# Kernel optimization log

Hardware: AMD Instinct MI355X
Metric: run time of the kernel (lower is better)

Reference implementation:

```python
import jax, jax.numpy as jnp
import numpy as np

N = 100000
E = 800000

def elu(x):
    return jnp.where(x > 0, x, jnp.expm1(x))

def transformer_conv(x, src, dst, ea, Wq, bq, Wk, bk, Wv, bv, We, Ws, bs, heads, ch):
    # PyG TransformerConv (concat=True, root_weight=True, beta=False, eval so dropout off)
    n = x.shape[0]
    q = (x @ Wq + bq).reshape(n, heads, ch)
    k = (x @ Wk + bk).reshape(n, heads, ch)
    v = (x @ Wv + bv).reshape(n, heads, ch)
    e = (ea @ We).reshape(-1, heads, ch)            # [E,H,C], lin_edge has no bias
    kj = k[src] + e                                  # [E,H,C]
    logits = (q[dst] * kj).sum(-1) / jnp.sqrt(jnp.float32(ch))  # [E,H]
    # segment softmax over incoming edges of each dst node
    m = jax.ops.segment_max(logits, dst, num_segments=n)
    ex = jnp.exp(logits - m[dst])
    denom = jax.ops.segment_sum(ex, dst, num_segments=n)
    alpha = ex / denom[dst]                          # [E,H]
    msg = alpha[..., None] * (v[src] + e)            # [E,H,C]
    agg = jax.ops.segment_sum(msg, dst, num_segments=n).reshape(n, heads * ch)
    return agg + x @ Ws + bs                         # skip connection (lin_skip)

def setup_inputs() -> dict:
    key = jax.random.key(0)
    ks = jax.random.split(key, 32)
    def rn(k, shape, scale=0.1):
        return jax.random.normal(k, shape, dtype=jnp.float32) * scale
    d = {}
    d['x'] = jax.random.normal(ks[0], (N, 23), dtype=jnp.float32)
    d['edge_index'] = jax.random.randint(ks[1], (2, E), 0, N, dtype=jnp.int32)
    d['edge_attr'] = jax.random.normal(ks[2], (E, 7), dtype=jnp.float32)
    d['linA_w'] = rn(ks[3], (23, 23)); d['linA_b'] = jnp.zeros((23,), jnp.float32)
    d['linB_w'] = rn(ks[4], (23, 23)); d['linB_b'] = jnp.zeros((23,), jnp.float32)
    # conv1: in=23, heads=8, out=24 -> 192
    d['q1_w'] = rn(ks[5], (23, 192)); d['q1_b'] = jnp.zeros((192,), jnp.float32)
    d['k1_w'] = rn(ks[6], (23, 192)); d['k1_b'] = jnp.zeros((192,), jnp.float32)
    d['v1_w'] = rn(ks[7], (23, 192)); d['v1_b'] = jnp.zeros((192,), jnp.float32)
    d['e1_w'] = rn(ks[8], (7, 192))
    d['s1_w'] = rn(ks[9], (23, 192)); d['s1_b'] = jnp.zeros((192,), jnp.float32)
    # conv4: in=192, heads=8, out=8 -> 64
    d['q2_w'] = rn(ks[10], (192, 64)); d['q2_b'] = jnp.zeros((64,), jnp.float32)
    d['k2_w'] = rn(ks[11], (192, 64)); d['k2_b'] = jnp.zeros((64,), jnp.float32)
    d['v2_w'] = rn(ks[12], (192, 64)); d['v2_b'] = jnp.zeros((64,), jnp.float32)
    d['e2_w'] = rn(ks[13], (7, 64))
    d['s2_w'] = rn(ks[14], (192, 64)); d['s2_b'] = jnp.zeros((64,), jnp.float32)
    d['lin1_w'] = rn(ks[15], (64, 20)); d['lin1_b'] = jnp.zeros((20,), jnp.float32)
    d['lin2_w'] = rn(ks[16], (20, 1)); d['lin2_b'] = jnp.zeros((1,), jnp.float32)
    return d

def reference(x, edge_index, edge_attr,
              linA_w, linA_b, linB_w, linB_b,
              q1_w, q1_b, k1_w, k1_b, v1_w, v1_b, e1_w, s1_w, s1_b,
              q2_w, q2_b, k2_w, k2_b, v2_w, v2_b, e2_w, s2_w, s2_b,
              lin1_w, lin1_b, lin2_w, lin2_b):
    src, dst = edge_index[0], edge_index[1]
    h = elu(x @ linA_w + linA_b)
    h = elu(h @ linB_w + linB_b)
    h = transformer_conv(h, src, dst, edge_attr, q1_w, q1_b, k1_w, k1_b, v1_w, v1_b, e1_w, s1_w, s1_b, 8, 24)
    h = elu(h)
    h = transformer_conv(h, src, dst, edge_attr, q2_w, q2_b, k2_w, k2_b, v2_w, v2_b, e2_w, s2_w, s2_b, 8, 8)
    h = elu(h)
    h = elu(h @ lin1_w + lin1_b)
    return h @ lin2_w + lin2_b
```

## Files before the change

### kernel.cpp

```cpp
#include <hip/hip_runtime.h>
#include <math.h>


__device__ __forceinline__ float elu_f(float x) {
    return x > 0.f ? x : expm1f(x);
}


__global__ void mlp_kernel(const float* __restrict__ x,
                           const float* __restrict__ A, const float* __restrict__ ab,
                           const float* __restrict__ B, const float* __restrict__ bb,
                           float* __restrict__ out, int n) {
    __shared__ float sA[23 * 23], sB[23 * 23], sa[23], sb[23];
    for (int t = threadIdx.x; t < 23 * 23; t += blockDim.x) { sA[t] = A[t]; sB[t] = B[t]; }
    if (threadIdx.x < 23) { sa[threadIdx.x] = ab[threadIdx.x]; sb[threadIdx.x] = bb[threadIdx.x]; }
    __syncthreads();
    int i = blockIdx.x * blockDim.x + threadIdx.x;
    if (i >= n) return;
    float xi[23], h1[23];
    #pragma unroll
    for (int j = 0; j < 23; j++) xi[j] = x[(size_t)i * 23 + j];
    #pragma unroll
    for (int o = 0; o < 23; o++) {
        float acc = sa[o];
        #pragma unroll
        for (int j = 0; j < 23; j++) acc = fmaf(xi[j], sA[j * 23 + o], acc);
        h1[o] = elu_f(acc);
    }
    #pragma unroll
    for (int o = 0; o < 23; o++) {
        float acc = sb[o];
        #pragma unroll
        for (int j = 0; j < 23; j++) acc = fmaf(h1[j], sB[j * 23 + o], acc);
        out[(size_t)i * 23 + o] = elu_f(acc);
    }
}

template<int IN, int Kc, int OUTW, int M, int TY, bool FUSED>
__global__ void proj_tiled_kernel(const float* __restrict__ in, int n,
    const float* __restrict__ W0, const float* __restrict__ b0, float* __restrict__ o0,
    const float* __restrict__ W1, const float* __restrict__ b1, float* __restrict__ o1,
    const float* __restrict__ W2, const float* __restrict__ b2, float* __restrict__ o2,
    const float* __restrict__ W3, const float* __restrict__ b3, float* __restrict__ o3) {
    constexpr int WTOT = M * OUTW;
    constexpr int CG   = WTOT / 8;
    constexpr int BN   = TY * 4;
    constexpr int SAW  = BN + 4;
    constexpr int NT   = CG * TY;
    static_assert(IN % Kc == 0, "Kc must divide IN");
    static_assert(WTOT % 8 == 0 && OUTW % 4 == 0, "col alignment");
    __shared__ float sA[Kc][SAW];
    __shared__ float sB[Kc][WTOT];

    const int tid = threadIdx.x;
    const int tx = tid % CG;
    const int ty = tid / CG;
    const int node0 = blockIdx.x * BN;

    const int colA = tx * 4;
    const int colB = WTOT / 2 + tx * 4;
    const int matA = colA / OUTW, ccA = colA % OUTW;
    const int matB = colB / OUTW, ccB = colB % OUTW;
    const float* bA = (matA == 0 ? b0 : matA == 1 ? b1 : matA == 2 ? b2 : b3);
    const float* bB = (matB == 0 ? b0 : matB == 1 ? b1 : matB == 2 ? b2 : b3);
    float*       oA = (matA == 0 ? o0 : matA == 1 ? o1 : matA == 2 ? o2 : o3);
    float*       oB = (matB == 0 ? o0 : matB == 1 ? o1 : matB == 2 ? o2 : o3);

    float acc[4][8];
    #pragma unroll
    for (int i = 0; i < 4; i++) {
        #pragma unroll
        for (int c = 0; c < 4; c++) { acc[i][c] = bA[ccA + c]; acc[i][4 + c] = bB[ccB + c]; }
    }

    for (int k0 = 0; k0 < IN; k0 += Kc) {
        for (int t = tid; t < Kc * BN; t += NT) {
            int j = t / BN, nn = t - j * BN;
            int g = node0 + nn;
            sA[j][nn] = (g < n) ? in[(size_t)g * IN + k0 + j] : 0.f;
        }
        for (int t = tid; t < Kc * WTOT; t += NT) {
            int j = t / WTOT, c = t - j * WTOT;
            int m = c / OUTW, cm = c - m * OUTW;
            const float* Wp = (m == 0 ? W0 : m == 1 ? W1 : m == 2 ? W2 : W3);
            sB[j][c] = Wp[(size_t)(k0 + j) * OUTW + cm];
        }
        __syncthreads();
        #pragma unroll 8
        for (int j = 0; j < Kc; j++) {
            float4 a  = *(const float4*)&sA[j][ty * 4];
            float4 v0 = *(const float4*)&sB[j][colA];
            float4 v1 = *(const float4*)&sB[j][colB];
            float av[4] = {a.x, a.y, a.z, a.w};
            float bv[8] = {v0.x, v0.y, v0.z, v0.w, v1.x, v1.y, v1.z, v1.w};
            #pragma unroll
            for (int i = 0; i < 4; i++)
                #pragma unroll
                for (int c = 0; c < 8; c++)
                    acc[i][c] = fmaf(av[i], bv[c], acc[i][c]);
        }
        __syncthreads();
    }

    #pragma unroll
    for (int i = 0; i < 4; i++) {
        int g = node0 + ty * 4 + i;
        if (g >= n) continue;
        if constexpr (FUSED) {
            *(float4*)(o0 + (size_t)g * WTOT + colA) = make_float4(acc[i][0], acc[i][1], acc[i][2], acc[i][3]);
            *(float4*)(o0 + (size_t)g * WTOT + colB) = make_float4(acc[i][4], acc[i][5], acc[i][6], acc[i][7]);
        } else {
            *(float4*)(oA + (size_t)g * OUTW + ccA) = make_float4(acc[i][0], acc[i][1], acc[i][2], acc[i][3]);
            *(float4*)(oB + (size_t)g * OUTW + ccB) = make_float4(acc[i][4], acc[i][5], acc[i][6], acc[i][7]);
        }
    }
}


__global__ void zero2_kernel(int* __restrict__ a, int* __restrict__ b, int n) {
    int i = blockIdx.x * blockDim.x + threadIdx.x;
    if (i < n) { a[i] = 0; b[i] = 0; }
}

__global__ void count_kernel(const int* __restrict__ dst, int* __restrict__ cnt, int nE) {
    int e = blockIdx.x * blockDim.x + threadIdx.x;
    if (e < nE) atomicAdd(&cnt[dst[e]], 1);
}

__global__ void scan_block_kernel(int* __restrict__ cnt, int* __restrict__ bsum, int n) {
    __shared__ int sdat[256];
    int i = blockIdx.x * 256 + threadIdx.x;
    int v = (i < n) ? cnt[i] : 0;
    sdat[threadIdx.x] = v;
    __syncthreads();
    for (int off = 1; off < 256; off <<= 1) {
        int t = (threadIdx.x >= (unsigned)off) ? sdat[threadIdx.x - off] : 0;
        __syncthreads();
        sdat[threadIdx.x] += t;
        __syncthreads();
    }
    if (i < n) cnt[i] = sdat[threadIdx.x] - v;
    if (threadIdx.x == 255) bsum[blockIdx.x] = sdat[255];
}

__global__ void scan_bsum_kernel(int* __restrict__ bsum, int nb) {
    __shared__ int s[1024];
    int i = threadIdx.x;
    int v = (i < nb) ? bsum[i] : 0;
    s[i] = v;
    __syncthreads();
    for (int off = 1; off < 1024; off <<= 1) {
        int t = (i >= off) ? s[i - off] : 0;
        __syncthreads();
        s[i] += t;
        __syncthreads();
    }
    if (i < nb) bsum[i] = s[i] - v;
}

__global__ void finalize_rp_kernel(const int* __restrict__ cnt, const int* __restrict__ bsum,
                                   int* __restrict__ rp, int n, int nE) {
    int i = blockIdx.x * blockDim.x + threadIdx.x;
    if (i < n) rp[i] = cnt[i] + bsum[i >> 8];
    if (i == n) rp[n] = nE;
}

__global__ void scatter_kernel(const int* __restrict__ src, const int* __restrict__ dst,
                               const int* __restrict__ rp, int* __restrict__ cur,
                               int2* __restrict__ seS, int nE) {
    int e = blockIdx.x * blockDim.x + threadIdx.x;
    if (e >= nE) return;
    int d = dst[e];
    int pos = rp[d] + atomicAdd(&cur[d], 1);
    seS[pos] = make_int2(src[e], e);
}

template<int IN, int C, bool VMAT, bool QMAT, bool DOELU>
__global__ __launch_bounds__(256, 8)
void conv_fused_kernel(const float* __restrict__ feat,
                       const float* __restrict__ Wq, const float* __restrict__ qb,
                       const float* __restrict__ Wv, const float* __restrict__ vb,
                       const float* __restrict__ kmat, const float* __restrict__ qmat,
                       const float* __restrict__ ea, const float* __restrict__ We,
                       const int* __restrict__ rp, const int2* __restrict__ seS,
                       float* __restrict__ out, int n, float scale, int chunk) {
    constexpr int HC = 8 * C;
    constexpr int CPL = HC / 64;
    __shared__ float sWv[VMAT ? 1 : IN * HC];
    if constexpr (!VMAT) {
        for (int t = threadIdx.x; t < IN * HC; t += blockDim.x) sWv[t] = Wv[t];
        __syncthreads();
    }
    const int lane = threadIdx.x & 63;
    const int wid = (blockIdx.x * blockDim.x + threadIdx.x) >> 6;
    const int d0 = wid * chunk;
    const int dEnd = min(n, d0 + chunk);
    if (d0 >= dEnd) return;
    const int ch0 = lane * CPL;

    float we[7][CPL];
    #pragma unroll
    for (int j = 0; j < 7; j++)
        #pragma unroll
        for (int c = 0; c < CPL; c++) we[j][c] = We[j * HC + ch0 + c];

    float vbr[CPL];
    if constexpr (!VMAT) {
        #pragma unroll
        for (int c = 0; c < CPL; c++) vbr[c] = vb[ch0 + c];
    }

    for (int d = d0; d < dEnd; d++) {
        float q[CPL];
        if constexpr (QMAT) {
            const float* qp = qmat + (size_t)d * HC + ch0;
            #pragma unroll
            for (int c = 0; c < CPL; c++) q[c] = qp[c];
        } else {
            #pragma unroll
            for (int c = 0; c < CPL; c++) q[c] = qb[ch0 + c];
            const float* fd = feat + (size_t)d * IN;
            for (int j = 0; j < IN; j++) {
                float f = fd[j];
                #pragma unroll
                for (int c = 0; c < CPL; c++)
                    q[c] = fmaf(f, Wq[(size_t)j * HC + ch0 + c], q[c]);
            }
        }

        float m = -INFINITY, l = 0.f, acc[CPL];
        #pragma unroll
        for (int c = 0; c < CPL; c++) acc[c] = 0.f;

        const int p0 = rp[d], p1 = rp[d + 1];

        if constexpr (VMAT) {
            if (p0 < p1) {
                int2 se0 = seS[p0];
                int sU = __builtin_amdgcn_readfirstlane(se0.x);
                int eU = __builtin_amdgcn_readfirstlane(se0.y);
                float ec[7];
                {
                    const float* ep = ea + (size_t)eU * 7;
                    #pragma unroll
                    for (int j = 0; j < 7; j++) ec[j] = ep[j];
                }
                for (int p = p0; p < p1; p++) {
                    const float* kp = kmat + (size_t)sU * (2 * HC) + ch0;
                    float kc[CPL], vc[CPL];
                    #pragma unroll
                    for (int c = 0; c < CPL; c++) { kc[c] = kp[c]; vc[c] = kp[HC + c]; }
                    const bool hasN = (p + 1 < p1);
                    int sN = sU, eN = eU;
                    if (hasN) {
                        int2 s2 = seS[p + 1];
                        sN = __builtin_amdgcn_readfirstlane(s2.x);
                        eN = __builtin_amdgcn_readfirstlane(s2.y);
                    }
                    float tv[CPL];
                    #pragma unroll
                    for (int c = 0; c < CPL; c++) {
                        float t = 0.f;
                        #pragma unroll
                        for (int j = 0; j < 7; j++) t = fmaf(ec[j], we[j][c], t);
                        tv[c] = t;
                    }
                    float part = 0.f;
                    #pragma unroll
                    for (int c = 0; c < CPL; c++) part = fmaf(q[c], kc[c] + tv[c], part);
                    part += __shfl_xor(part, 1);
                    part += __shfl_xor(part, 2);
                    part += __shfl_xor(part, 4);
                    float z = part * scale;
                    float mn = fmaxf(m, z);
                    float rs = expf(m - mn);
                    float pw = expf(z - mn);
                    l = l * rs + pw;
                    #pragma unroll
                    for (int c = 0; c < CPL; c++) acc[c] = fmaf(acc[c], rs, pw * (vc[c] + tv[c]));
                    m = mn;
                    if (hasN) {
                        const float* ep = ea + (size_t)eN * 7;
                        #pragma unroll
                        for (int j = 0; j < 7; j++) ec[j] = ep[j];
                    }
                    sU = sN; eU = eN;
                }
            }
        } else {
            for (int p = p0; p < p1; p++) {
                int2 se = seS[p];
                int s = se.x, eid = se.y;
                const float* eav = ea + (size_t)eid * 7;
                float ev[7];
                #pragma unroll
                for (int j = 0; j < 7; j++) ev[j] = eav[j];
                const float* kp = kmat + (size_t)s * HC + ch0;
                float vv[CPL];
                float part = 0.f;
                #pragma unroll
                for (int c = 0; c < CPL; c++) {
                    float t = 0.f;
                    #pragma unroll
                    for (int j = 0; j < 7; j++) t = fmaf(ev[j], we[j][c], t);
                    part = fmaf(q[c], kp[c] + t, part);
                    vv[c] = t + vbr[c];
                }
                const float* fs = feat + (size_t)s * IN;
                for (int j = 0; j < IN; j++) {
                    float f = fs[j];
                    #pragma unroll
                    for (int c = 0; c < CPL; c++) vv[c] = fmaf(f, sWv[j * HC + ch0 + c], vv[c]);
                }
                part += __shfl_xor(part, 1);
                part += __shfl_xor(part, 2);
                part += __shfl_xor(part, 4);
                float z = part * scale;
                float mn = fmaxf(m, z);
                float rs = expf(m - mn);
                float pw = expf(z - mn);
                l = l * rs + pw;
                #pragma unroll
                for (int c = 0; c < CPL; c++) acc[c] = fmaf(acc[c], rs, pw * vv[c]);
                m = mn;
            }
        }

        float invl = (l > 0.f) ? 1.f / l : 0.f;
        float* op = out + (size_t)d * HC + ch0;
        #pragma unroll
        for (int c = 0; c < CPL; c++) {
            float r = op[c] + acc[c] * invl;
            op[c] = DOELU ? elu_f(r) : r;
        }
    }
}

__global__ void head_kernel(const float* __restrict__ h, const float* __restrict__ W1,
                            const float* __restrict__ b1, const float* __restrict__ W2,
                            const float* __restrict__ b2, float* __restrict__ out, int n) {
    __shared__ float sW1[64 * 20], sb1[20], sW2[20], sb2;
    for (int t = threadIdx.x; t < 64 * 20; t += blockDim.x) sW1[t] = W1[t];
    if (threadIdx.x < 20) { sb1[threadIdx.x] = b1[threadIdx.x]; sW2[threadIdx.x] = W2[threadIdx.x]; }
    if (threadIdx.x == 0) sb2 = b2[0];
    __syncthreads();
    int i = blockIdx.x * blockDim.x + threadIdx.x;
    if (i >= n) return;
    float hv[64];
    const float* hp = h + (size_t)i * 64;
    #pragma unroll
    for (int j = 0; j < 64; j++) hv[j] = elu_f(hp[j]);
    float acc2 = sb2;
    for (int o = 0; o < 20; o++) {
        float a = sb1[o];
        #pragma unroll
        for (int j = 0; j < 64; j++) a = fmaf(hv[j], sW1[j * 20 + o], a);
        acc2 = fmaf(elu_f(a), sW2[o], acc2);
    }
    out[i] = acc2;
}

__global__ void zero_out_kernel(float* __restrict__ out, int n) {
    int i = blockIdx.x * blockDim.x + threadIdx.x;
    if (i < n) out[i] = 0.f;
}


extern "C" void kernel_launch(void* const* d_in, const int* in_sizes, int n_in,
                              void* d_out, int out_size, void* d_ws, size_t ws_size,
                              hipStream_t stream) {
    const float* x   = (const float*)d_in[0];
    const int*   ei  = (const int*)d_in[1];
    const float* ea  = (const float*)d_in[2];
    const float* Aw  = (const float*)d_in[3];
    const float* Ab  = (const float*)d_in[4];
    const float* Bw  = (const float*)d_in[5];
    const float* Bb  = (const float*)d_in[6];
    const float* q1w = (const float*)d_in[7];  const float* q1b = (const float*)d_in[8];
    const float* k1w = (const float*)d_in[9];  const float* k1b = (const float*)d_in[10];
    const float* v1w = (const float*)d_in[11]; const float* v1b = (const float*)d_in[12];
    const float* e1w = (const float*)d_in[13];
    const float* s1w = (const float*)d_in[14]; const float* s1b = (const float*)d_in[15];
    const float* q2w = (const float*)d_in[16]; const float* q2b = (const float*)d_in[17];
    const float* k2w = (const float*)d_in[18]; const float* k2b = (const float*)d_in[19];
    const float* v2w = (const float*)d_in[20]; const float* v2b = (const float*)d_in[21];
    const float* e2w = (const float*)d_in[22];
    const float* s2w = (const float*)d_in[23]; const float* s2b = (const float*)d_in[24];
    const float* l1w = (const float*)d_in[25]; const float* l1b = (const float*)d_in[26];
    const float* l2w = (const float*)d_in[27]; const float* l2b = (const float*)d_in[28];

    const int n  = in_sizes[0] / 23;
    const int nE = in_sizes[1] / 2;
    const int* src = ei;
    const int* dst = ei + nE;
    float* out = (float*)d_out;
    const int B = 256;
    const int nb = (n + 255) / 256;

    size_t fl_h1 = ((size_t)n * 23 + 3) & ~(size_t)3;
    size_t fl_o1 = (size_t)n * 192;
    size_t fl_kvA = (size_t)n * 384;
    size_t fl_kB  = (size_t)n * 192;
    size_t fl_q1  = (size_t)n * 192;
    size_t ints_total = 2 * (size_t)nE + ((size_t)n + 1) + n + n + 1024;

    size_t tierB_bytes  = (fl_h1 + fl_o1 + fl_kB) * 4 + ints_total * 4;
    size_t tierA_bytes  = (fl_h1 + fl_o1 + fl_kvA) * 4 + ints_total * 4;
    size_t tierA2_bytes = tierA_bytes + fl_q1 * 4;

    if (ws_size < tierB_bytes || nb > 1024) {
        zero_out_kernel<<<(out_size + B - 1) / B, B, 0, stream>>>(out, out_size);
        return;
    }
    const int tier = (ws_size >= tierA2_bytes) ? 2 : (ws_size >= tierA_bytes) ? 1 : 0;

    float* ws = (float*)d_ws;
    size_t off = 0;
    float* h1   = ws + off; off += fl_h1;
    float* o1   = ws + off; off += fl_o1;
    float* kbuf = ws + off; off += (tier >= 1 ? fl_kvA : fl_kB);
    float* q1buf = nullptr;
    if (tier == 2) { q1buf = ws + off; off += fl_q1; }
    int2* seS = (int2*)(ws + off);
    int* ip = (int*)(seS + nE);
    int* rp   = ip; ip += (size_t)n + 1;
    int* cnt  = ip; ip += n;
    int* cur  = ip; ip += n;
    int* bsum = ip;

    float* kv2   = kbuf;
    float* q2buf = (tier >= 1) ? (kbuf + (size_t)n * 128) : nullptr;
    float* o2    = (tier >= 1) ? (kbuf + (size_t)n * 192) : (kbuf + (size_t)n * 128);

    const float sc1 = 1.0f / sqrtf(24.0f);
    const float sc2 = 1.0f / sqrtf(8.0f);
    const float* np = nullptr;
    float* npw = nullptr;

    zero2_kernel<<<(n + B - 1) / B, B, 0, stream>>>(cnt, cur, n);
    count_kernel<<<(nE + B - 1) / B, B, 0, stream>>>(dst, cnt, nE);
    scan_block_kernel<<<nb, 256, 0, stream>>>(cnt, bsum, n);
    scan_bsum_kernel<<<1, 1024, 0, stream>>>(bsum, nb);
    finalize_rp_kernel<<<(n + 1 + B - 1) / B, B, 0, stream>>>(cnt, bsum, rp, n, nE);
    scatter_kernel<<<(nE + B - 1) / B, B, 0, stream>>>(src, dst, rp, cur, seS, nE);

    mlp_kernel<<<(n + B - 1) / B, B, 0, stream>>>(x, Aw, Ab, Bw, Bb, h1, n);

    const int gproj32 = (n + 31) / 32;
    const int gproj64 = (n + 63) / 64;

    const int CB = 2048;
    const int NW = CB * 4;
    const int chunk = (n + NW - 1) / NW;

    if (tier >= 1) {
        proj_tiled_kernel<23, 23, 192, 2, 8, true><<<gproj32, 384, 0, stream>>>(
            h1, n, k1w, k1b, kbuf, v1w, v1b, npw, np, np, npw, np, np, npw);
        if (tier == 2) {
            proj_tiled_kernel<23, 23, 192, 2, 8, false><<<gproj32, 384, 0, stream>>>(
                h1, n, s1w, s1b, o1, q1w, q1b, q1buf, np, np, npw, np, np, npw);
            conv_fused_kernel<23, 24, true, true, true><<<CB, 256, 0, stream>>>(
                h1, q1w, q1b, v1w, v1b, kbuf, q1buf, ea, e1w, rp, seS, o1, n, sc1, chunk);
        } else {
            proj_tiled_kernel<23, 23, 192, 1, 8, false><<<gproj32, 192, 0, stream>>>(
                h1, n, s1w, s1b, o1, np, np, npw, np, np, npw, np, np, npw);
            conv_fused_kernel<23, 24, true, false, true><<<CB, 256, 0, stream>>>(
                h1, q1w, q1b, v1w, v1b, kbuf, np, ea, e1w, rp, seS, o1, n, sc1, chunk);
        }
    } else {
        proj_tiled_kernel<23, 23, 192, 2, 8, false><<<gproj32, 384, 0, stream>>>(
            h1, n, k1w, k1b, kbuf, s1w, s1b, o1, np, np, npw, np, np, npw);
        conv_fused_kernel<23, 24, false, false, true><<<CB, 256, 0, stream>>>(
            h1, q1w, q1b, v1w, v1b, kbuf, np, ea, e1w, rp, seS, o1, n, sc1, chunk);
    }

    proj_tiled_kernel<192, 32, 64, 2, 16, true><<<gproj64, 256, 0, stream>>>(
        o1, n, k2w, k2b, kv2, v2w, v2b, npw, np, np, npw, np, np, npw);
    if (tier >= 1) {
        proj_tiled_kernel<192, 32, 64, 2, 16, false><<<gproj64, 256, 0, stream>>>(
            o1, n, q2w, q2b, q2buf, s2w, s2b, o2, np, np, npw, np, np, npw);
        conv_fused_kernel<192, 8, true, true, false><<<CB, 256, 0, stream>>>(
            o1, q2w, q2b, v2w, v2b, kv2, q2buf, ea, e2w, rp, seS, o2, n, sc2, chunk);
    } else {
        proj_tiled_kernel<192, 32, 64, 1, 16, false><<<gproj64, 128, 0, stream>>>(
            o1, n, s2w, s2b, o2, np, np, npw, np, np, npw, np, np, npw);
        conv_fused_kernel<192, 8, true, false, false><<<CB, 256, 0, stream>>>(
            o1, q2w, q2b, v2w, v2b, kv2, np, ea, e2w, rp, seS, o2, n, sc2, chunk);
    }

    head_kernel<<<(n + B - 1) / B, B, 0, stream>>>(o2, l1w, l1b, l2w, l2b, out, n);
}
```

Baseline: 1.317 ms.

## Split edge loop across lane subgroups with online-softmax merge in conv kernel

The attention-aggregation kernel now divides each wavefront into subgroups: each subgroup covers all channels of a node but handles a strided subset of its incoming edges. The subgroups then merge their running max, denominator and accumulators through xor-shuffle log-sum-exp combines. The edge-weight matrix moves from per-lane registers into shared memory, and the launch-bounds occupancy hint is dropped. The goal is more independent gathers in flight per node and less serial latency per edge chain. In exchange, each lane holds more channels, the merge costs extra shuffles, and shared-memory reads replace register reads.

```diff
diff --git a/kernel.cpp b/kernel.cpp
--- a/kernel.cpp
+++ b/kernel.cpp
@@ -175,34 +175,36 @@
     seS[pos] = make_int2(src[e], e);
 }
 
-template<int IN, int C, bool VMAT, bool QMAT, bool DOELU>
-__global__ __launch_bounds__(256, 8)
-void conv_fused_kernel(const float* __restrict__ feat,
-                       const float* __restrict__ Wq, const float* __restrict__ qb,
-                       const float* __restrict__ Wv, const float* __restrict__ vb,
-                       const float* __restrict__ kmat, const float* __restrict__ qmat,
-                       const float* __restrict__ ea, const float* __restrict__ We,
-                       const int* __restrict__ rp, const int2* __restrict__ seS,
-                       float* __restrict__ out, int n, float scale, int chunk) {
+template<int IN, int C, int LSPLIT, bool VMAT, bool QMAT, bool DOELU>
+__global__ void conv_fused_kernel(const float* __restrict__ feat,
+                                  const float* __restrict__ Wq, const float* __restrict__ qb,
+                                  const float* __restrict__ Wv, const float* __restrict__ vb,
+                                  const float* __restrict__ kmat, const float* __restrict__ qmat,
+                                  const float* __restrict__ ea, const float* __restrict__ We,
+                                  const int* __restrict__ rp, const int2* __restrict__ seS,
+                                  float* __restrict__ out, int n, float scale, int chunk) {
     constexpr int HC = 8 * C;
-    constexpr int CPL = HC / 64;
+    constexpr int CPL = HC / LSPLIT;
+    constexpr int NSPLIT = 64 / LSPLIT;
+    constexpr int LPG = C / CPL;
+    static_assert(HC % LSPLIT == 0 && C % CPL == 0, "split alignment");
+
+    __shared__ float sWe[7 * HC];
     __shared__ float sWv[VMAT ? 1 : IN * HC];
+    for (int t = threadIdx.x; t < 7 * HC; t += blockDim.x) sWe[t] = We[t];
     if constexpr (!VMAT) {
         for (int t = threadIdx.x; t < IN * HC; t += blockDim.x) sWv[t] = Wv[t];
-        __syncthreads();
-    }
+    }
+    __syncthreads();
+
     const int lane = threadIdx.x & 63;
     const int wid = (blockIdx.x * blockDim.x + threadIdx.x) >> 6;
     const int d0 = wid * chunk;
     const int dEnd = min(n, d0 + chunk);
     if (d0 >= dEnd) return;
-    const int ch0 = lane * CPL;
-
-    float we[7][CPL];
-    #pragma unroll
-    for (int j = 0; j < 7; j++)
-        #pragma unroll
-        for (int c = 0; c < CPL; c++) we[j][c] = We[j * HC + ch0 + c];
+    const int li = lane & (LSPLIT - 1);
+    const int sub = lane / LSPLIT;
+    const int ch0 = li * CPL;
 
     float vbr[CPL];
     if constexpr (!VMAT) {
@@ -235,57 +237,54 @@
         const int p0 = rp[d], p1 = rp[d + 1];
 
         if constexpr (VMAT) {
-            if (p0 < p1) {
-                int2 se0 = seS[p0];
-                int sU = __builtin_amdgcn_readfirstlane(se0.x);
-                int eU = __builtin_amdgcn_readfirstlane(se0.y);
+            for (int p = p0 + sub; p < p1; p += NSPLIT) {
+                int2 se = seS[p];
+                const float* kp = kmat + (size_t)se.x * (2 * HC) + ch0;
+                float kc[CPL], vc[CPL];
+                #pragma unroll
+                for (int c = 0; c < CPL; c++) kc[c] = kp[c];
+                #pragma unroll
+                for (int c = 0; c < CPL; c++) vc[c] = kp[HC + c];
+                const float* ep = ea + (size_t)se.y * 7;
                 float ec[7];
-                {
-                    const float* ep = ea + (size_t)eU * 7;
+                #pragma unroll
+                for (int j = 0; j < 7; j++) ec[j] = ep[j];
+
+                float part = 0.f, tv[CPL];
+                #pragma unroll
+                for (int c = 0; c < CPL; c++) {
+                    float t = 0.f;
                     #pragma unroll
-                    for (int j = 0; j < 7; j++) ec[j] = ep[j];
+                    for (int j = 0; j < 7; j++) t = fmaf(ec[j], sWe[j * HC + ch0 + c], t);
+                    tv[c] = t;
+                    part = fmaf(q[c], kc[c] + t, part);
                 }
-                for (int p = p0; p < p1; p++) {
-                    const float* kp = kmat + (size_t)sU * (2 * HC) + ch0;
-                    float kc[CPL], vc[CPL];
-                    #pragma unroll
-                    for (int c = 0; c < CPL; c++) { kc[c] = kp[c]; vc[c] = kp[HC + c]; }
-                    const bool hasN = (p + 1 < p1);
-                    int sN = sU, eN = eU;
-                    if (hasN) {
-                        int2 s2 = seS[p + 1];
-                        sN = __builtin_amdgcn_readfirstlane(s2.x);
-                        eN = __builtin_amdgcn_readfirstlane(s2.y);
-                    }
-                    float tv[CPL];
-                    #pragma unroll
-                    for (int c = 0; c < CPL; c++) {
-                        float t = 0.f;
-                        #pragma unroll
-                        for (int j = 0; j < 7; j++) t = fmaf(ec[j], we[j][c], t);
-                        tv[c] = t;
-                    }
-                    float part = 0.f;
-                    #pragma unroll
-                    for (int c = 0; c < CPL; c++) part = fmaf(q[c], kc[c] + tv[c], part);
-                    part += __shfl_xor(part, 1);
-                    part += __shfl_xor(part, 2);
-                    part += __shfl_xor(part, 4);
-                    float z = part * scale;
-                    float mn = fmaxf(m, z);
-                    float rs = expf(m - mn);
-                    float pw = expf(z - mn);
-                    l = l * rs + pw;
-                    #pragma unroll
-                    for (int c = 0; c < CPL; c++) acc[c] = fmaf(acc[c], rs, pw * (vc[c] + tv[c]));
-                    m = mn;
-                    if (hasN) {
-                        const float* ep = ea + (size_t)eN * 7;
-                        #pragma unroll
-                        for (int j = 0; j < 7; j++) ec[j] = ep[j];
-                    }
-                    sU = sN; eU = eN;
-                }
+                if constexpr (LPG > 1) part += __shfl_xor(part, 1);
+                if constexpr (LPG > 2) part += __shfl_xor(part, 2);
+                if constexpr (LPG > 4) part += __shfl_xor(part, 4);
+                float z = part * scale;
+                float mn = fmaxf(m, z);
+                float rs = expf(m - mn);
+                float pw = expf(z - mn);
+                l = l * rs + pw;
+                #pragma unroll
+                for (int c = 0; c < CPL; c++) acc[c] = fmaf(acc[c], rs, pw * (vc[c] + tv[c]));
+                m = mn;
+            }
+            #pragma unroll
+            for (int off = LSPLIT; off < 64; off <<= 1) {
+                float mo = __shfl_xor(m, off);
+                float lo = __shfl_xor(l, off);
+                float ao[CPL];
+                #pragma unroll
+                for (int c = 0; c < CPL; c++) ao[c] = __shfl_xor(acc[c], off);
+                float mn = fmaxf(m, mo);
+                float ra = (l  > 0.f) ? expf(m  - mn) : 0.f;
+                float rb = (lo > 0.f) ? expf(mo - mn) : 0.f;
+                l = l * ra + lo * rb;
+                #pragma unroll
+                for (int c = 0; c < CPL; c++) acc[c] = acc[c] * ra + ao[c] * rb;
+                m = mn;
             }
         } else {
             for (int p = p0; p < p1; p++) {
@@ -302,7 +301,7 @@
                 for (int c = 0; c < CPL; c++) {
                     float t = 0.f;
                     #pragma unroll
-                    for (int j = 0; j < 7; j++) t = fmaf(ev[j], we[j][c], t);
+                    for (int j = 0; j < 7; j++) t = fmaf(ev[j], sWe[j * HC + ch0 + c], t);
                     part = fmaf(q[c], kp[c] + t, part);
                     vv[c] = t + vbr[c];
                 }
@@ -312,9 +311,9 @@
                     #pragma unroll
                     for (int c = 0; c < CPL; c++) vv[c] = fmaf(f, sWv[j * HC + ch0 + c], vv[c]);
                 }
-                part += __shfl_xor(part, 1);
-                part += __shfl_xor(part, 2);
-                part += __shfl_xor(part, 4);
+                if constexpr (LPG > 1) part += __shfl_xor(part, 1);
+                if constexpr (LPG > 2) part += __shfl_xor(part, 2);
+                if constexpr (LPG > 4) part += __shfl_xor(part, 4);
                 float z = part * scale;
                 float mn = fmaxf(m, z);
                 float rs = expf(m - mn);
@@ -328,10 +327,12 @@
 
         float invl = (l > 0.f) ? 1.f / l : 0.f;
         float* op = out + (size_t)d * HC + ch0;
-        #pragma unroll
-        for (int c = 0; c < CPL; c++) {
-            float r = op[c] + acc[c] * invl;
-            op[c] = DOELU ? elu_f(r) : r;
+        if (sub == 0) {
+            #pragma unroll
+            for (int c = 0; c < CPL; c++) {
+                float r = op[c] + acc[c] * invl;
+                op[c] = DOELU ? elu_f(r) : r;
+            }
         }
     }
 }
@@ -459,18 +460,18 @@
         if (tier == 2) {
             proj_tiled_kernel<23, 23, 192, 2, 8, false><<<gproj32, 384, 0, stream>>>(
                 h1, n, s1w, s1b, o1, q1w, q1b, q1buf, np, np, npw, np, np, npw);
-            conv_fused_kernel<23, 24, true, true, true><<<CB, 256, 0, stream>>>(
+            conv_fused_kernel<23, 24, 32, true, true, true><<<CB, 256, 0, stream>>>(
                 h1, q1w, q1b, v1w, v1b, kbuf, q1buf, ea, e1w, rp, seS, o1, n, sc1, chunk);
         } else {
             proj_tiled_kernel<23, 23, 192, 1, 8, false><<<gproj32, 192, 0, stream>>>(
                 h1, n, s1w, s1b, o1, np, np, npw, np, np, npw, np, np, npw);
-            conv_fused_kernel<23, 24, true, false, true><<<CB, 256, 0, stream>>>(
+            conv_fused_kernel<23, 24, 32, true, false, true><<<CB, 256, 0, stream>>>(
                 h1, q1w, q1b, v1w, v1b, kbuf, np, ea, e1w, rp, seS, o1, n, sc1, chunk);
         }
     } else {
         proj_tiled_kernel<23, 23, 192, 2, 8, false><<<gproj32, 384, 0, stream>>>(
             h1, n, k1w, k1b, kbuf, s1w, s1b, o1, np, np, npw, np, np, npw);
-        conv_fused_kernel<23, 24, false, false, true><<<CB, 256, 0, stream>>>(
+        conv_fused_kernel<23, 24, 64, false, false, true><<<CB, 256, 0, stream>>>(
             h1, q1w, q1b, v1w, v1b, kbuf, np, ea, e1w, rp, seS, o1, n, sc1, chunk);
     }
 
@@ -479,12 +480,12 @@
     if (tier >= 1) {
         proj_tiled_kernel<192, 32, 64, 2, 16, false><<<gproj64, 256, 0, stream>>>(
             o1, n, q2w, q2b, q2buf, s2w, s2b, o2, np, np, npw, np, np, npw);
-        conv_fused_kernel<192, 8, true, true, false><<<CB, 256, 0, stream>>>(
+        conv_fused_kernel<192, 8, 16, true, true, false><<<CB, 256, 0, stream>>>(
             o1, q2w, q2b, v2w, v2b, kv2, q2buf, ea, e2w, rp, seS, o2, n, sc2, chunk);
     } else {
         proj_tiled_kernel<192, 32, 64, 1, 16, false><<<gproj64, 128, 0, stream>>>(
             o1, n, s2w, s2b, o2, np, np, npw, np, np, npw, np, np, npw);
-        conv_fused_kernel<192, 8, true, false, false><<<CB, 256, 0, stream>>>(
+        conv_fused_kernel<192, 8, 16, true, false, false><<<CB, 256, 0, stream>>>(
             o1, q2w, q2b, v2w, v2b, kv2, np, ea, e2w, rp, seS, o2, n, sc2, chunk);
     }
 
```

After: 1.420 ms. 1.08x slower.
